# Kernel tuning notes

Hardware: AMD Instinct MI355X
Metric: run time of the kernel (lower is better)

Reference implementation:

```python
import jax, jax.numpy as jnp
import numpy as np

INPUT_DIM = 1024
HIDDEN_DIM = 1024
OUTPUT_DIM = 1024
NUM_HEADS = 16
HEAD_DIM = HIDDEN_DIM // NUM_HEADS


def setup_inputs() -> dict:
    key = jax.random.key(0)
    ks = jax.random.split(key, 9)
    s = 1.0 / np.sqrt(INPUT_DIM)
    so = 1.0 / np.sqrt(HIDDEN_DIM)
    x = jax.random.normal(ks[0], (4, 2048, INPUT_DIM), dtype=jnp.float32)
    Wq = jax.random.uniform(ks[1], (INPUT_DIM, HIDDEN_DIM), minval=-s, maxval=s, dtype=jnp.float32)
    bq = jax.random.uniform(ks[2], (HIDDEN_DIM,), minval=-s, maxval=s, dtype=jnp.float32)
    Wk = jax.random.uniform(ks[3], (INPUT_DIM, HIDDEN_DIM), minval=-s, maxval=s, dtype=jnp.float32)
    bk = jax.random.uniform(ks[4], (HIDDEN_DIM,), minval=-s, maxval=s, dtype=jnp.float32)
    Wv = jax.random.uniform(ks[5], (INPUT_DIM, HIDDEN_DIM), minval=-s, maxval=s, dtype=jnp.float32)
    bv = jax.random.uniform(ks[6], (HIDDEN_DIM,), minval=-s, maxval=s, dtype=jnp.float32)
    Wo = jax.random.uniform(ks[7], (HIDDEN_DIM, OUTPUT_DIM), minval=-so, maxval=so, dtype=jnp.float32)
    bo = jax.random.uniform(ks[8], (OUTPUT_DIM,), minval=-so, maxval=so, dtype=jnp.float32)
    return {"x": x, "Wq": Wq, "bq": bq, "Wk": Wk, "bk": bk, "Wv": Wv, "bv": bv, "Wo": Wo, "bo": bo}


def reference(x, Wq, bq, Wk, bk, Wv, bv, Wo, bo):
    B, S, _ = x.shape
    H, D = NUM_HEADS, HEAD_DIM
    # project and split heads -> [B, H, S, D]
    Q = (x @ Wq + bq).reshape(B, S, H, D).transpose(0, 2, 1, 3)
    K = (x @ Wk + bk).reshape(B, S, H, D).transpose(0, 2, 1, 3)
    V = (x @ Wv + bv).reshape(B, S, H, D).transpose(0, 2, 1, 3)
    scores = jnp.einsum('bhsd,bhtd->bhst', Q, K) / jnp.sqrt(jnp.asarray(D, x.dtype))
    attn = jax.nn.softmax(scores, axis=-1)
    out = jnp.einsum('bhst,bhtd->bhsd', attn, V)  # [B, H, S, D]
    out = out.transpose(0, 2, 1, 3).reshape(B, S, H * D)
    return out @ Wo + bo
```

## Files before the change

kernel.cpp:

```cpp
#include <hip/hip_runtime.h>

#define DI __device__ __forceinline__

typedef __bf16 bf16x8 __attribute__((ext_vector_type(8)));
typedef float f32x4 __attribute__((ext_vector_type(4)));
typedef float f32x16 __attribute__((ext_vector_type(16)));
typedef unsigned u32;
typedef u32 u32x2v __attribute__((ext_vector_type(2)));
typedef u32 u32x4v __attribute__((ext_vector_type(4)));

#define QSCALE 0.180336880111f

DI ushort f2bf(float f) {
  unsigned u = __builtin_bit_cast(unsigned, f);
  unsigned r = (u + 0x7FFFu + ((u >> 16) & 1u)) >> 16;
  return (ushort)r;
}

DI void gload_lds16(const void* g, void* l) {
  __builtin_amdgcn_global_load_lds(
      (const __attribute__((address_space(1))) unsigned*)g,
      (__attribute__((address_space(3))) unsigned*)l, 16, 0, 0);
}

DI bf16x8 load_frag(const ushort* p) { return *(const bf16x8*)p; }

DI u32 cvtpk(float lo, float hi) {
  u32 r;
  asm("v_cvt_pk_bf16_f32 %0, %1, %2" : "=v"(r) : "v"(lo), "v"(hi));
  return r;
}

#if defined(__has_builtin)
#if __has_builtin(__builtin_amdgcn_permlane32_swap)
#define HAVE_PLSWAP 1
#endif
#endif

DI u32x2v permswap(u32 a, u32 b) {
#ifdef HAVE_PLSWAP
  return __builtin_amdgcn_permlane32_swap(a, b, false, false);
#else
  int hi = (threadIdx.x >> 5) & 1;
  u32 bl = __shfl_xor(b, 32, 64);
  u32 ah = __shfl_xor(a, 32, 64);
  u32x2v r;
  r[0] = hi ? bl : a;
  r[1] = hi ? b : ah;
  return r;
#endif
}

DI f32x16 mfma32(bf16x8 a, bf16x8 b, f32x16 c) {
  return __builtin_amdgcn_mfma_f32_32x32x16_bf16(a, b, c, 0, 0, 0);
}

__global__ __launch_bounds__(256) void k_convert_x(const float* __restrict__ x,
                                                   ushort* __restrict__ xb) {
  int i = (blockIdx.x * 256 + threadIdx.x) * 4;
  float4 v = *(const float4*)(x + i);
  ushort4 o;
  o.x = f2bf(v.x); o.y = f2bf(v.y); o.z = f2bf(v.z); o.w = f2bf(v.w);
  *(ushort4*)(xb + i) = o;
}

__global__ __launch_bounds__(256) void k_transpose_w4(
    const float* __restrict__ W0, const float* __restrict__ W1,
    const float* __restrict__ W2, const float* __restrict__ W3,
    ushort* __restrict__ T0, ushort* __restrict__ T1,
    ushort* __restrict__ T2, ushort* __restrict__ T3) {
  __shared__ float tile[64][65];
  int which = blockIdx.x >> 8;
  int bt = blockIdx.x & 255;
  const float* W = which == 0 ? W0 : which == 1 ? W1 : which == 2 ? W2 : W3;
  ushort* Wt = which == 0 ? T0 : which == 1 ? T1 : which == 2 ? T2 : T3;
  int k0 = (bt & 15) << 6;
  int n0 = (bt >> 4) << 6;
  int c = threadIdx.x & 63;
  int r0 = threadIdx.x >> 6;
#pragma unroll
  for (int i = 0; i < 16; ++i) {
    int r = i * 4 + r0;
    tile[r][c] = W[(k0 + r) * 1024 + n0 + c];
  }
  __syncthreads();
#pragma unroll
  for (int i = 0; i < 16; ++i) {
    int nn = i * 4 + r0;
    Wt[(n0 + nn) * 1024 + k0 + c] = f2bf(tile[c][nn]);
  }
}

__global__ __launch_bounds__(256, 2) void k_gemm_qkv(
    const ushort* __restrict__ A, const ushort* __restrict__ Bt3,
    const float* __restrict__ bq, const float* __restrict__ bk,
    const float* __restrict__ bv, ushort* __restrict__ Qb,
    ushort* __restrict__ Kb, ushort* __restrict__ Vtb) {
  __shared__ ushort Asm[8192];
  __shared__ ushort Bsm[8192];
  int L = blockIdx.x;
  int wg = (L & 7) * 192 + (L >> 3);
  int brow = wg / 24;
  int bcol = wg % 24;
  int which = bcol >> 3;
  int colb = bcol & 7;
  int tid = threadIdx.x;
  int w = tid >> 6, lane = tid & 63;
  int g = lane >> 4, lr = lane & 15;
  int wr = w >> 1, wc = w & 1;
  const char* Abase = (const char*)(A + (size_t)brow * 128 * 1024);
  const char* Bbase = (const char*)(Bt3 + (size_t)bcol * 128 * 1024);
  f32x4 acc[4][4] = {};
  for (int kt = 0; kt < 16; ++kt) {
    int k0b = kt * 128;
#pragma unroll
    for (int i = 0; i < 4; ++i) {
      int j = w * 4 + i;
      int fo = j * 1024 + lane * 16;
      int row = fo >> 7;
      int cis = ((fo >> 4) & 7) ^ (row & 7);
      long srcoff = (long)row * 2048 + k0b + cis * 16;
      gload_lds16(Abase + srcoff, (char*)Asm + j * 1024);
      gload_lds16(Bbase + srcoff, (char*)Bsm + j * 1024);
    }
    __syncthreads();
#pragma unroll
    for (int ks = 0; ks < 2; ++ks) {
      bf16x8 af[4], bfr[4];
#pragma unroll
      for (int m = 0; m < 4; ++m) {
        int row = wr * 64 + m * 16 + lr;
        int ci = (ks * 4 + g) ^ (row & 7);
        af[m] = *(const bf16x8*)((const char*)Asm + row * 128 + ci * 16);
      }
#pragma unroll
      for (int n = 0; n < 4; ++n) {
        int row = wc * 64 + n * 16 + lr;
        int ci = (ks * 4 + g) ^ (row & 7);
        bfr[n] = *(const bf16x8*)((const char*)Bsm + row * 128 + ci * 16);
      }
#pragma unroll
      for (int m = 0; m < 4; ++m)
#pragma unroll
        for (int n = 0; n < 4; ++n)
          acc[m][n] = __builtin_amdgcn_mfma_f32_16x16x32_bf16(af[m], bfr[n], acc[m][n], 0, 0, 0);
    }
    __syncthreads();
  }
  const float* bp = which == 0 ? bq : which == 1 ? bk : bv;
  float osc = which == 0 ? QSCALE : 1.0f;
#pragma unroll
  for (int m = 0; m < 4; ++m) {
#pragma unroll
    for (int n = 0; n < 4; ++n) {
      int c = colb * 128 + wc * 64 + n * 16 + lr;
      float bvv = bp[c];
      int h = c >> 6, d = c & 63;
#pragma unroll
      for (int r = 0; r < 4; ++r) {
        int R = brow * 128 + wr * 64 + m * 16 + g * 4 + r;
        int b = R >> 11, s = R & 2047;
        float v = (acc[m][n][r] + bvv) * osc;
        if (which == 0)
          Qb[(((size_t)(b * 16 + h) * 2048 + s) << 6) + d] = f2bf(v);
        else if (which == 1)
          Kb[(((size_t)(b * 16 + h) * 2048 + s) << 6) + d] = f2bf(v);
        else
          Vtb[(((size_t)(b * 16 + h) * 64 + d) << 11) + s] = f2bf(v);
      }
    }
  }
}

__global__ __launch_bounds__(256, 2) void k_gemm_o(const ushort* __restrict__ A,
                                                   const ushort* __restrict__ Bt,
                                                   const float* __restrict__ bias,
                                                   float* __restrict__ out) {
  __shared__ ushort Asm[8192];
  __shared__ ushort Bsm[8192];
  int L = blockIdx.x;
  int wg = (L & 7) * 64 + (L >> 3);
  int brow = wg >> 3;
  int bcol = wg & 7;
  int tid = threadIdx.x;
  int w = tid >> 6, lane = tid & 63;
  int g = lane >> 4, lr = lane & 15;
  int wr = w >> 1, wc = w & 1;
  const char* Abase = (const char*)(A + (size_t)brow * 128 * 1024);
  const char* Bbase = (const char*)(Bt + (size_t)bcol * 128 * 1024);
  f32x4 acc[4][4] = {};
  for (int kt = 0; kt < 16; ++kt) {
    int k0b = kt * 128;
#pragma unroll
    for (int i = 0; i < 4; ++i) {
      int j = w * 4 + i;
      int fo = j * 1024 + lane * 16;
      int row = fo >> 7;
      int cis = ((fo >> 4) & 7) ^ (row & 7);
      long srcoff = (long)row * 2048 + k0b + cis * 16;
      gload_lds16(Abase + srcoff, (char*)Asm + j * 1024);
      gload_lds16(Bbase + srcoff, (char*)Bsm + j * 1024);
    }
    __syncthreads();
#pragma unroll
    for (int ks = 0; ks < 2; ++ks) {
      bf16x8 af[4], bfr[4];
#pragma unroll
      for (int m = 0; m < 4; ++m) {
        int row = wr * 64 + m * 16 + lr;
        int ci = (ks * 4 + g) ^ (row & 7);
        af[m] = *(const bf16x8*)((const char*)Asm + row * 128 + ci * 16);
      }
#pragma unroll
      for (int n = 0; n < 4; ++n) {
        int row = wc * 64 + n * 16 + lr;
        int ci = (ks * 4 + g) ^ (row & 7);
        bfr[n] = *(const bf16x8*)((const char*)Bsm + row * 128 + ci * 16);
      }
#pragma unroll
      for (int m = 0; m < 4; ++m)
#pragma unroll
        for (int n = 0; n < 4; ++n)
          acc[m][n] = __builtin_amdgcn_mfma_f32_16x16x32_bf16(af[m], bfr[n], acc[m][n], 0, 0, 0);
    }
    __syncthreads();
  }
#pragma unroll
  for (int m = 0; m < 4; ++m) {
#pragma unroll
    for (int n = 0; n < 4; ++n) {
      int Cc = bcol * 128 + wc * 64 + n * 16 + lr;
      float bvv = bias[Cc];
#pragma unroll
      for (int r = 0; r < 4; ++r) {
        int R = brow * 128 + wr * 64 + m * 16 + g * 4 + r;
        out[(size_t)R * 1024 + Cc] = acc[m][n][r] + bvv;
      }
    }
  }
}

DI void stage2(const char* Kp, const char* Vp, char* Kd, char* Vd, int t0,
               int w, int lane) {
#pragma unroll
  for (int i = 0; i < 2; ++i) {
    int j = w * 2 + i;
    int fo = j * 1024 + lane * 16;
    int row = fo >> 7;
    int ch = ((fo >> 4) & 7) ^ (row & 7);
    gload_lds16(Kp + (size_t)(t0 + row) * 128 + ch * 16, Kd + j * 1024);
    gload_lds16(Vp + (size_t)row * 4096 + (size_t)t0 * 2 + ch * 16, Vd + j * 1024);
  }
}

#define PACKP(pp, base, dst)                                \
  {                                                         \
    u32 a0 = cvtpk(pp[(base) + 0], pp[(base) + 1]);         \
    u32 b0 = cvtpk(pp[(base) + 4], pp[(base) + 5]);         \
    u32 a1 = cvtpk(pp[(base) + 2], pp[(base) + 3]);         \
    u32 b1 = cvtpk(pp[(base) + 6], pp[(base) + 7]);         \
    u32x2v r0 = permswap(a0, b0);                           \
    u32x2v r1 = permswap(a1, b1);                           \
    u32x4v f;                                               \
    f.x = r0.x; f.y = r1.x; f.z = r0.y; f.w = r1.y;         \
    dst = __builtin_bit_cast(bf16x8, f);                    \
  }

__global__ __launch_bounds__(256, 4) void k_attn(const ushort* __restrict__ Qb,
                                                 const ushort* __restrict__ Kb,
                                                 const ushort* __restrict__ Vt,
                                                 ushort* __restrict__ aout) {
  __shared__ ushort Ksm[2][4096];
  __shared__ ushort Vsm[2][4096];
  int L = blockIdx.x;
  int xcd = L & 7, idx = L >> 3;
  int bh = xcd * 8 + (idx >> 4);
  int qt = idx & 15;
  int b = bh >> 4, h = bh & 15;
  int tid = threadIdx.x;
  int w = tid >> 6, lane = tid & 63, l31 = lane & 31, hi = lane >> 5;
  const ushort* Qp = Qb + (size_t)bh * 2048 * 64;
  const char* Kp = (const char*)(Kb + (size_t)bh * 2048 * 64);
  const char* Vp = (const char*)(Vt + (size_t)bh * 64 * 2048);

  int q0 = qt * 128 + w * 32;
  bf16x8 qf[4];
#pragma unroll
  for (int ks = 0; ks < 4; ++ks)
    qf[ks] = load_frag(Qp + (q0 + l31) * 64 + ks * 16 + hi * 8);
  f32x16 o0 = {}, o1 = {};
  float ssum[16];
#pragma unroll
  for (int i = 0; i < 16; ++i) ssum[i] = 0.f;

  stage2(Kp, Vp, (char*)Ksm[0], (char*)Vsm[0], 0, w, lane);
  __syncthreads();
  int cur = 0;
#pragma unroll 2
  for (int t = 0; t < 32; ++t) {
    if (t < 31)
      stage2(Kp, Vp, (char*)Ksm[cur ^ 1], (char*)Vsm[cur ^ 1], (t + 1) * 64, w, lane);
    const char* Kc = (const char*)Ksm[cur];
    const char* Vc = (const char*)Vsm[cur];
    f32x16 s0 = {}, s1 = {};
#pragma unroll
    for (int ks = 0; ks < 4; ++ks) {
      int ci = ((ks * 2 + hi) ^ (l31 & 7)) << 4;
      bf16x8 ka0 = *(const bf16x8*)(Kc + l31 * 128 + ci);
      bf16x8 ka1 = *(const bf16x8*)(Kc + (32 + l31) * 128 + ci);
      s0 = mfma32(ka0, qf[ks], s0);
      s1 = mfma32(ka1, qf[ks], s1);
    }
    float p0[16], p1[16];
#pragma unroll
    for (int i = 0; i < 16; ++i) {
      p0[i] = __builtin_amdgcn_exp2f(s0[i]);
      p1[i] = __builtin_amdgcn_exp2f(s1[i]);
    }
#pragma unroll
    for (int i = 0; i < 16; ++i) ssum[i] += p0[i] + p1[i];
    bf16x8 pb0, pb1, pb2, pb3;
    PACKP(p0, 0, pb0);
    PACKP(p0, 8, pb1);
    PACKP(p1, 0, pb2);
    PACKP(p1, 8, pb3);
#pragma unroll
    for (int ks = 0; ks < 4; ++ks) {
      int ci = ((ks * 2 + hi) ^ (l31 & 7)) << 4;
      bf16x8 va0 = *(const bf16x8*)(Vc + l31 * 128 + ci);
      bf16x8 va1 = *(const bf16x8*)(Vc + (32 + l31) * 128 + ci);
      bf16x8 pb = (ks == 0) ? pb0 : (ks == 1) ? pb1 : (ks == 2) ? pb2 : pb3;
      o0 = mfma32(va0, pb, o0);
      o1 = mfma32(va1, pb, o1);
    }
    __syncthreads();
    cur ^= 1;
  }
#pragma unroll
  for (int st = 8; st >= 1; st >>= 1)
#pragma unroll
    for (int i = 0; i < st; ++i) ssum[i] += ssum[i + st];
  float lsum = ssum[0] + __shfl_xor(ssum[0], 32, 64);
  float rl = 1.f / lsum;
  ushort* orow = aout + ((size_t)b * 2048 + q0 + l31) * 1024 + h * 64;
#pragma unroll
  for (int r = 0; r < 8; ++r) {
    int d0 = ((2 * r) & 3) + 8 * ((2 * r) >> 2) + 4 * hi;
    *(u32*)(orow + d0) = cvtpk(o0[2 * r] * rl, o0[2 * r + 1] * rl);
    *(u32*)(orow + 32 + d0) = cvtpk(o1[2 * r] * rl, o1[2 * r + 1] * rl);
  }
}

extern "C" void kernel_launch(void* const* d_in, const int* in_sizes, int n_in,
                              void* d_out, int out_size, void* d_ws, size_t ws_size,
                              hipStream_t stream) {
  const float* x  = (const float*)d_in[0];
  const float* Wq = (const float*)d_in[1];
  const float* bq = (const float*)d_in[2];
  const float* Wk = (const float*)d_in[3];
  const float* bk = (const float*)d_in[4];
  const float* Wv = (const float*)d_in[5];
  const float* bv = (const float*)d_in[6];
  const float* Wo = (const float*)d_in[7];
  const float* bo = (const float*)d_in[8];
  char* wsb = (char*)d_ws;
  ushort* xb   = (ushort*)(wsb);
  ushort* WqT  = (ushort*)(wsb + (16u << 20));
  ushort* WkT  = (ushort*)(wsb + (18u << 20));
  ushort* WvT  = (ushort*)(wsb + (20u << 20));
  ushort* WoT  = (ushort*)(wsb + (22u << 20));
  ushort* Qb   = (ushort*)(wsb + (24u << 20));
  ushort* Kb   = (ushort*)(wsb + (40u << 20));
  ushort* Vtb  = (ushort*)(wsb + (56u << 20));
  ushort* aout = xb;

  k_convert_x<<<8192, 256, 0, stream>>>(x, xb);
  k_transpose_w4<<<1024, 256, 0, stream>>>(Wq, Wk, Wv, Wo, WqT, WkT, WvT, WoT);
  k_gemm_qkv<<<1536, 256, 0, stream>>>(xb, WqT, bq, bk, bv, Qb, Kb, Vtb);
  k_attn<<<1024, 256, 0, stream>>>(Qb, Kb, Vtb, aout);
  k_gemm_o<<<512, 256, 0, stream>>>(aout, WoT, bo, (float*)d_out);
}
```

Measured before the change: 306.3 us.

## Double query rows per wave in attention with triple-buffered K/V and tile swizzles

The attention kernel now gives each wave 64 query rows instead of 32, so every K/V LDS fragment feeds two MFMAs. The grid is halved to 512 blocks and occupancy lowered to 2. K/V staging moves from double to triple buffering with a partial vmcnt wait and one barrier per iteration, and s_setprio is raised around the MFMA sections. Both GEMMs also remap blocks so each XCD gets an 8x8 group of tiles for better L2 reuse. The cost is higher register pressure and fewer resident waves.

Measured after the change: 263.2 us. -14.1%, faster.

```diff
diff --git a/kernel.cpp b/kernel.cpp
--- a/kernel.cpp
+++ b/kernel.cpp
@@ -99,9 +99,12 @@
   __shared__ ushort Asm[8192];
   __shared__ ushort Bsm[8192];
   int L = blockIdx.x;
-  int wg = (L & 7) * 192 + (L >> 3);
-  int brow = wg / 24;
-  int bcol = wg % 24;
+  int xcd = L & 7;
+  int i0 = L >> 3;
+  int chunk = i0 >> 6;
+  int j = i0 & 63;
+  int brow = xcd * 8 + (j & 7);
+  int bcol = chunk * 8 + (j >> 3);
   int which = bcol >> 3;
   int colb = bcol & 7;
   int tid = threadIdx.x;
@@ -115,13 +118,13 @@
     int k0b = kt * 128;
 #pragma unroll
     for (int i = 0; i < 4; ++i) {
-      int j = w * 4 + i;
-      int fo = j * 1024 + lane * 16;
+      int jj = w * 4 + i;
+      int fo = jj * 1024 + lane * 16;
       int row = fo >> 7;
       int cis = ((fo >> 4) & 7) ^ (row & 7);
       long srcoff = (long)row * 2048 + k0b + cis * 16;
-      gload_lds16(Abase + srcoff, (char*)Asm + j * 1024);
-      gload_lds16(Bbase + srcoff, (char*)Bsm + j * 1024);
+      gload_lds16(Abase + srcoff, (char*)Asm + jj * 1024);
+      gload_lds16(Bbase + srcoff, (char*)Bsm + jj * 1024);
     }
     __syncthreads();
 #pragma unroll
@@ -179,9 +182,10 @@
   __shared__ ushort Asm[8192];
   __shared__ ushort Bsm[8192];
   int L = blockIdx.x;
-  int wg = (L & 7) * 64 + (L >> 3);
-  int brow = wg >> 3;
-  int bcol = wg & 7;
+  int xcd = L & 7;
+  int j = L >> 3;
+  int brow = xcd * 8 + (j & 7);
+  int bcol = j >> 3;
   int tid = threadIdx.x;
   int w = tid >> 6, lane = tid & 63;
   int g = lane >> 4, lr = lane & 15;
@@ -193,13 +197,13 @@
     int k0b = kt * 128;
 #pragma unroll
     for (int i = 0; i < 4; ++i) {
-      int j = w * 4 + i;
-      int fo = j * 1024 + lane * 16;
+      int jj = w * 4 + i;
+      int fo = jj * 1024 + lane * 16;
       int row = fo >> 7;
       int cis = ((fo >> 4) & 7) ^ (row & 7);
       long srcoff = (long)row * 2048 + k0b + cis * 16;
-      gload_lds16(Abase + srcoff, (char*)Asm + j * 1024);
-      gload_lds16(Bbase + srcoff, (char*)Bsm + j * 1024);
+      gload_lds16(Abase + srcoff, (char*)Asm + jj * 1024);
+      gload_lds16(Bbase + srcoff, (char*)Bsm + jj * 1024);
     }
     __syncthreads();
 #pragma unroll
@@ -266,16 +270,16 @@
     dst = __builtin_bit_cast(bf16x8, f);                    \
   }
 
-__global__ __launch_bounds__(256, 4) void k_attn(const ushort* __restrict__ Qb,
+__global__ __launch_bounds__(256, 2) void k_attn(const ushort* __restrict__ Qb,
                                                  const ushort* __restrict__ Kb,
                                                  const ushort* __restrict__ Vt,
                                                  ushort* __restrict__ aout) {
-  __shared__ ushort Ksm[2][4096];
-  __shared__ ushort Vsm[2][4096];
+  __shared__ ushort Ksm[3][4096];
+  __shared__ ushort Vsm[3][4096];
   int L = blockIdx.x;
   int xcd = L & 7, idx = L >> 3;
-  int bh = xcd * 8 + (idx >> 4);
-  int qt = idx & 15;
+  int bh = xcd * 8 + (idx >> 3);
+  int qt = idx & 7;
   int b = bh >> 4, h = bh & 15;
   int tid = threadIdx.x;
   int w = tid >> 6, lane = tid & 63, l31 = lane & 31, hi = lane >> 5;
@@ -283,71 +287,100 @@
   const char* Kp = (const char*)(Kb + (size_t)bh * 2048 * 64);
   const char* Vp = (const char*)(Vt + (size_t)bh * 64 * 2048);
 
-  int q0 = qt * 128 + w * 32;
-  bf16x8 qf[4];
-#pragma unroll
-  for (int ks = 0; ks < 4; ++ks)
-    qf[ks] = load_frag(Qp + (q0 + l31) * 64 + ks * 16 + hi * 8);
-  f32x16 o0 = {}, o1 = {};
-  float ssum[16];
-#pragma unroll
-  for (int i = 0; i < 16; ++i) ssum[i] = 0.f;
-
-  stage2(Kp, Vp, (char*)Ksm[0], (char*)Vsm[0], 0, w, lane);
-  __syncthreads();
-  int cur = 0;
-#pragma unroll 2
+  int q0 = qt * 256 + w * 64;
+  bf16x8 qf0[4], qf1[4];
+#pragma unroll
+  for (int ks = 0; ks < 4; ++ks) {
+    qf0[ks] = load_frag(Qp + (q0 + l31) * 64 + ks * 16 + hi * 8);
+    qf1[ks] = load_frag(Qp + (q0 + 32 + l31) * 64 + ks * 16 + hi * 8);
+  }
+  f32x16 o00 = {}, o01 = {}, o10 = {}, o11 = {};
+  f32x16 sum0 = {}, sum1 = {};
+
+  char *kA = (char*)Ksm[0], *kB = (char*)Ksm[1], *kC = (char*)Ksm[2];
+  char *vA = (char*)Vsm[0], *vB = (char*)Vsm[1], *vC = (char*)Vsm[2];
+  stage2(Kp, Vp, kA, vA, 0, w, lane);
+  stage2(Kp, Vp, kB, vB, 64, w, lane);
+
   for (int t = 0; t < 32; ++t) {
-    if (t < 31)
-      stage2(Kp, Vp, (char*)Ksm[cur ^ 1], (char*)Vsm[cur ^ 1], (t + 1) * 64, w, lane);
-    const char* Kc = (const char*)Ksm[cur];
-    const char* Vc = (const char*)Vsm[cur];
-    f32x16 s0 = {}, s1 = {};
+    asm volatile("s_waitcnt vmcnt(4)" ::: "memory");
+    __builtin_amdgcn_s_barrier();
+    int nt = t + 2;
+    if (nt >= 32) nt -= 32;
+    stage2(Kp, Vp, kC, vC, nt * 64, w, lane);
+    const char* Kc = kA;
+    const char* Vc = vA;
+    f32x16 s00 = {}, s01 = {};
+    __builtin_amdgcn_s_setprio(1);
 #pragma unroll
     for (int ks = 0; ks < 4; ++ks) {
       int ci = ((ks * 2 + hi) ^ (l31 & 7)) << 4;
-      bf16x8 ka0 = *(const bf16x8*)(Kc + l31 * 128 + ci);
-      bf16x8 ka1 = *(const bf16x8*)(Kc + (32 + l31) * 128 + ci);
-      s0 = mfma32(ka0, qf[ks], s0);
-      s1 = mfma32(ka1, qf[ks], s1);
-    }
-    float p0[16], p1[16];
+      bf16x8 ka = *(const bf16x8*)(Kc + l31 * 128 + ci);
+      s00 = mfma32(ka, qf0[ks], s00);
+      s01 = mfma32(ka, qf1[ks], s01);
+    }
+    __builtin_amdgcn_s_setprio(0);
 #pragma unroll
     for (int i = 0; i < 16; ++i) {
-      p0[i] = __builtin_amdgcn_exp2f(s0[i]);
-      p1[i] = __builtin_amdgcn_exp2f(s1[i]);
-    }
-#pragma unroll
-    for (int i = 0; i < 16; ++i) ssum[i] += p0[i] + p1[i];
-    bf16x8 pb0, pb1, pb2, pb3;
-    PACKP(p0, 0, pb0);
-    PACKP(p0, 8, pb1);
-    PACKP(p1, 0, pb2);
-    PACKP(p1, 8, pb3);
+      s00[i] = __builtin_amdgcn_exp2f(s00[i]);
+      s01[i] = __builtin_amdgcn_exp2f(s01[i]);
+      sum0[i] += s00[i];
+      sum1[i] += s01[i];
+    }
+    bf16x8 pA0, pA1, pA2, pA3, pB0, pB1, pB2, pB3;
+    PACKP(s00, 0, pA0); PACKP(s00, 8, pA1);
+    PACKP(s01, 0, pB0); PACKP(s01, 8, pB1);
+    f32x16 s10 = {}, s11 = {};
+    __builtin_amdgcn_s_setprio(1);
+#pragma unroll
+    for (int ks = 0; ks < 4; ++ks) {
+      int ci = ((ks * 2 + hi) ^ (l31 & 7)) << 4;
+      bf16x8 ka = *(const bf16x8*)(Kc + (32 + l31) * 128 + ci);
+      s10 = mfma32(ka, qf0[ks], s10);
+      s11 = mfma32(ka, qf1[ks], s11);
+    }
+    __builtin_amdgcn_s_setprio(0);
+#pragma unroll
+    for (int i = 0; i < 16; ++i) {
+      s10[i] = __builtin_amdgcn_exp2f(s10[i]);
+      s11[i] = __builtin_amdgcn_exp2f(s11[i]);
+      sum0[i] += s10[i];
+      sum1[i] += s11[i];
+    }
+    PACKP(s10, 0, pA2); PACKP(s10, 8, pA3);
+    PACKP(s11, 0, pB2); PACKP(s11, 8, pB3);
+    __builtin_amdgcn_s_setprio(1);
 #pragma unroll
     for (int ks = 0; ks < 4; ++ks) {
       int ci = ((ks * 2 + hi) ^ (l31 & 7)) << 4;
       bf16x8 va0 = *(const bf16x8*)(Vc + l31 * 128 + ci);
       bf16x8 va1 = *(const bf16x8*)(Vc + (32 + l31) * 128 + ci);
-      bf16x8 pb = (ks == 0) ? pb0 : (ks == 1) ? pb1 : (ks == 2) ? pb2 : pb3;
-      o0 = mfma32(va0, pb, o0);
-      o1 = mfma32(va1, pb, o1);
-    }
-    __syncthreads();
-    cur ^= 1;
-  }
-#pragma unroll
-  for (int st = 8; st >= 1; st >>= 1)
-#pragma unroll
-    for (int i = 0; i < st; ++i) ssum[i] += ssum[i + st];
-  float lsum = ssum[0] + __shfl_xor(ssum[0], 32, 64);
-  float rl = 1.f / lsum;
-  ushort* orow = aout + ((size_t)b * 2048 + q0 + l31) * 1024 + h * 64;
+      bf16x8 pa = (ks == 0) ? pA0 : (ks == 1) ? pA1 : (ks == 2) ? pA2 : pA3;
+      bf16x8 pb = (ks == 0) ? pB0 : (ks == 1) ? pB1 : (ks == 2) ? pB2 : pB3;
+      o00 = mfma32(va0, pa, o00);
+      o10 = mfma32(va1, pa, o10);
+      o01 = mfma32(va0, pb, o01);
+      o11 = mfma32(va1, pb, o11);
+    }
+    __builtin_amdgcn_s_setprio(0);
+    char* tk = kA; kA = kB; kB = kC; kC = tk;
+    char* tv = vA; vA = vB; vB = vC; vC = tv;
+  }
+  float ls0 = 0.f, ls1 = 0.f;
+#pragma unroll
+  for (int i = 0; i < 16; ++i) { ls0 += sum0[i]; ls1 += sum1[i]; }
+  ls0 += __shfl_xor(ls0, 32, 64);
+  ls1 += __shfl_xor(ls1, 32, 64);
+  float rl0 = 1.f / ls0, rl1 = 1.f / ls1;
+  ushort* orow0 = aout + ((size_t)b * 2048 + q0 + l31) * 1024 + h * 64;
+  ushort* orow1 = aout + ((size_t)b * 2048 + q0 + 32 + l31) * 1024 + h * 64;
 #pragma unroll
   for (int r = 0; r < 8; ++r) {
     int d0 = ((2 * r) & 3) + 8 * ((2 * r) >> 2) + 4 * hi;
-    *(u32*)(orow + d0) = cvtpk(o0[2 * r] * rl, o0[2 * r + 1] * rl);
-    *(u32*)(orow + 32 + d0) = cvtpk(o1[2 * r] * rl, o1[2 * r + 1] * rl);
+    *(u32*)(orow0 + d0)      = cvtpk(o00[2 * r] * rl0, o00[2 * r + 1] * rl0);
+    *(u32*)(orow0 + 32 + d0) = cvtpk(o10[2 * r] * rl0, o10[2 * r + 1] * rl0);
+    *(u32*)(orow1 + d0)      = cvtpk(o01[2 * r] * rl1, o01[2 * r + 1] * rl1);
+    *(u32*)(orow1 + 32 + d0) = cvtpk(o11[2 * r] * rl1, o11[2 * r + 1] * rl1);
   }
 }
 
@@ -377,6 +410,6 @@
   k_convert_x<<<8192, 256, 0, stream>>>(x, xb);
   k_transpose_w4<<<1024, 256, 0, stream>>>(Wq, Wk, Wv, Wo, WqT, WkT, WvT, WoT);
   k_gemm_qkv<<<1536, 256, 0, stream>>>(xb, WqT, bq, bk, bv, Qb, Kb, Vtb);
-  k_attn<<<1024, 256, 0, stream>>>(Qb, Kb, Vtb, aout);
+  k_attn<<<512, 256, 0, stream>>>(Qb, Kb, Vtb, aout);
   k_gemm_o<<<512, 256, 0, stream>>>(aout, WoT, bo, (float*)d_out);
 }
```
